# Kernel tuning notes

Hardware: AMD Instinct MI355X
Metric: run time of the kernel (lower is better)

The kernel has to match this reference:

```python
import jax, jax.numpy as jnp
import numpy as np

SIGMA_DATA = 16.0
ALPHA_BOND = 1.0


def safe_norm(x, axis=-1):
    # L2 norm with zero (sub)gradient at 0, matching torch.norm's behavior
    sq = jnp.sum(x * x, axis=axis)
    n = jnp.sqrt(jnp.where(sq > 0, sq, 1.0))
    return jnp.where(sq > 0, n, 0.0)


def weighted_rigid_align(x_l, xGT_l, w_l):
    # Aligns x_l onto xGT_l's frame (Kabsch with weights); output is detached.
    wm = w_l[..., None]                                   # [B,N,1]
    denom = jnp.sum(wm, axis=1, keepdims=True)
    mu = jnp.sum(wm * x_l, axis=1, keepdims=True) / denom
    muGT = jnp.sum(wm * xGT_l, axis=1, keepdims=True) / denom
    xc = x_l - mu
    xGTc = xGT_l - muGT
    # M = (w * xGT_c)^T @ x_c  -> [B,3,3]
    M = jnp.einsum('bni,bnj->bij', wm * xGTc, xc)
    U, S, Vh = jnp.linalg.svd(M)
    R = U @ Vh
    det = jnp.linalg.det(R)
    Fm = jnp.array([[1.0, 0.0, 0.0], [0.0, 1.0, 0.0], [0.0, 0.0, -1.0]], dtype=R.dtype)
    Rfix = jnp.einsum('bij,jk,bkl->bil', U, Fm, Vh)
    R = jnp.where(det[:, None, None] < 0, Rfix, R)
    xalign = xc @ jnp.swapaxes(R, -1, -2) + muGT
    return jax.lax.stop_gradient(xalign)


def diffusion_loss(xpred_l, xGT_l, ht, w_l):
    # Align ground truth onto prediction (note arg order in original forward)
    xGT_aligned = weighted_rigid_align(xGT_l, xpred_l, w_l)
    loss = jnp.sum(safe_norm(xpred_l - xGT_aligned) * w_l) / jnp.sum(w_l)
    if ALPHA_BOND > 0:
        w_pair = w_l[:, :, None] * w_l[:, None, :]                 # [B,N,N]
        d_pred = safe_norm(xpred_l[:, :, None] - xpred_l[:, None]) # [B,N,N]
        d_gt = safe_norm(xGT_l[:, :, None] - xGT_l[:, None])       # [B,N,N]
        L_bond = w_pair * (d_pred - d_gt) ** 2
        loss = loss + ALPHA_BOND * jnp.sum(L_bond) / jnp.sum(w_pair)
    return (ht ** 2 + SIGMA_DATA ** 2) / (ht + SIGMA_DATA) ** 2 * loss


def setup_inputs() -> dict:
    key = jax.random.key(0)
    k1, k2, k3, k4 = jax.random.split(key, 4)
    B, N = 4, 2048
    xpred_l = jax.random.normal(k1, (B, N, 3), dtype=jnp.float32) * 10.0
    xGT_l = jax.random.normal(k2, (B, N, 3), dtype=jnp.float32) * 10.0
    ht = jax.random.uniform(k3, (B,), dtype=jnp.float32, minval=0.1, maxval=4.0)
    w_l = jax.random.uniform(k4, (B, N), dtype=jnp.float32, minval=0.1, maxval=1.0)
    return {"xpred_l": xpred_l, "xGT_l": xGT_l, "ht": ht, "w_l": w_l}


def reference(xpred_l, xGT_l, ht, w_l):
    return diffusion_loss(xpred_l, xGT_l, ht, w_l)
```

## Files before the change

kernel.cpp:

```cpp
#include <hip/hip_runtime.h>
#include <math.h>


#define RT 256
#define TR 128
#define TC 128
#define MAXB 8

__global__ __launch_bounds__(RT, 4)
void k_bond_stats(const float* __restrict__ pred, const float* __restrict__ gt,
                  const float* __restrict__ w, double* __restrict__ ws,
                  int N, int B, int T, int CTILES, unsigned total) {
    const int b    = blockIdx.y;
    const int tid  = threadIdx.x;
    const int lane = tid & 63, wave = tid >> 6;

    int rem = blockIdx.x, bx = 0;
    while (rem >= CTILES - bx) { rem -= (CTILES - bx); bx++; }
    const int by = bx + rem;
    const int r0 = bx * TR, c0 = by * TC;

    double* statsSlot = ws;
    double* bondSlot  = ws + (size_t)B * CTILES * 16;
    if (blockIdx.x == 0 && blockIdx.y == 0 && tid == 0) {
        double* fin = bondSlot + total;
        fin[0] = 0.0; fin[1] = 0.0; fin[2] = 0.0;
    }

    const float* p  = pred + (size_t)b * N * 3;
    const float* g  = gt   + (size_t)b * N * 3;
    const float* wb = w    + (size_t)b * N;

    __shared__ float4 sp4[TC], sg4[TC];
    __shared__ double shred[4][16];

    const int rrow  = tid & (TR - 1);
    const int rhalf = tid >> 7;
    const int n     = r0 + rrow;
    const bool row_ok = (n < N);
    float px=0.f,py=0.f,pz=0.f,gx=0.f,gy=0.f,gz=0.f,wn=0.f;
    if (row_ok) {
        px = p[3*n]; py = p[3*n+1]; pz = p[3*n+2];
        gx = g[3*n]; gy = g[3*n+1]; gz = g[3*n+2];
        wn = wb[n];
    }

    {
        int i = tid & (TC - 1);
        int m = c0 + i;
        if (tid < TC) {
            float4 v = make_float4(0.f,0.f,0.f,0.f);
            if (m < N) v = make_float4(p[3*m], p[3*m+1], p[3*m+2], wb[m]);
            sp4[i] = v;
        } else {
            float4 v = make_float4(0.f,0.f,0.f,0.f);
            if (m < N) v = make_float4(g[3*m], g[3*m+1], g[3*m+2], 0.f);
            sg4[i] = v;
        }
    }
    __syncthreads();

    float acc = 0.f;
    const int ib = rhalf * (TC / 2);
    if (by > bx) {
        #pragma unroll 4
        for (int j = 0; j < TC/2; j++) {
            int i = ib + j;
            float4 cp = sp4[i], cg = sg4[i];
            float dxp=px-cp.x, dyp=py-cp.y, dzp=pz-cp.z;
            float dxg=gx-cg.x, dyg=gy-cg.y, dzg=gz-cg.z;
            float dp = sqrtf(dxp*dxp+dyp*dyp+dzp*dzp);
            float dg = sqrtf(dxg*dxg+dyg*dyg+dzg*dzg);
            float dd = dp - dg;
            acc = fmaf(cp.w, dd*dd, acc);
        }
    } else {
        #pragma unroll 4
        for (int j = 0; j < TC/2; j++) {
            int i = ib + j;
            float4 cp = sp4[i], cg = sg4[i];
            float dxp=px-cp.x, dyp=py-cp.y, dzp=pz-cp.z;
            float dxg=gx-cg.x, dyg=gy-cg.y, dzg=gz-cg.z;
            float dp = sqrtf(dxp*dxp+dyp*dyp+dzp*dzp);
            float dg = sqrtf(dxg*dxg+dyg*dyg+dzg*dzg);
            float dd = dp - dg;
            float t  = cp.w * (dd*dd);
            acc += (i > rrow) ? t : 0.f;
        }
    }
    float bond_f = 2.0f * wn * acc;

    if (bx == by) {
        double wd = (rhalf == 0) ? (double)wn : 0.0;
        double pxd=px,pyd=py,pzd=pz, gxd=gx,gyd=gy,gzd=gz;
        double st[16] = {wd, wd*pxd, wd*pyd, wd*pzd, wd*gxd, wd*gyd, wd*gzd,
                         wd*pxd*gxd, wd*pxd*gyd, wd*pxd*gzd,
                         wd*pyd*gxd, wd*pyd*gyd, wd*pyd*gzd,
                         wd*pzd*gxd, wd*pzd*gyd, wd*pzd*gzd};
        #pragma unroll
        for (int off = 32; off > 0; off >>= 1) {
            #pragma unroll
            for (int k = 0; k < 16; k++) st[k] += __shfl_down(st[k], off, 64);
        }
        if (lane == 0) {
            #pragma unroll
            for (int k = 0; k < 16; k++) shred[wave][k] = st[k];
        }
        __syncthreads();
        if (tid < 16)
            statsSlot[((size_t)b*CTILES + bx)*16 + tid] =
                shred[0][tid]+shred[1][tid]+shred[2][tid]+shred[3][tid];
        __syncthreads();
    }

    double bd = (double)bond_f;
    #pragma unroll
    for (int off = 32; off > 0; off >>= 1) bd += __shfl_down(bd, off, 64);
    if (lane == 0) shred[wave][0] = bd;
    __syncthreads();
    if (tid == 0)
        bondSlot[(size_t)blockIdx.y * T + blockIdx.x] =
            shred[0][0]+shred[1][0]+shred[2][0]+shred[3][0];
}

__global__ __launch_bounds__(RT, 1)
void k_tail2(const float* __restrict__ pred, const float* __restrict__ gt,
             const float* __restrict__ ht, const float* __restrict__ w,
             float* __restrict__ out, double* __restrict__ ws,
             int N, int B, int GX, unsigned total, int AG) {
    const int tid  = threadIdx.x;
    const int lane = tid & 63, wave = tid >> 6;
    const double* statsSlot = ws;
    const double* bondSlot  = ws + (size_t)B * GX * 16;
    double* fin = (double*)(bondSlot + total);

    __shared__ double sstat[MAXB][16];
    __shared__ float  sR[MAXB][15];
    __shared__ double sW[MAXB];
    __shared__ double shredA[4], shredB[4];

    float htv[MAXB];
    if (tid == 0) {
        #pragma unroll
        for (int b2 = 0; b2 < MAXB; b2++) htv[b2] = (b2 < B) ? ht[b2] : 0.f;
    }

    if (tid < B * 16) {
        int bb = tid >> 4, k = tid & 15;
        double acc = 0.0;
        for (int j = 0; j < GX; j++) acc += statsSlot[((size_t)bb*GX + j)*16 + k];
        sstat[bb][k] = acc;
    }

    double bsum = 0.0;
    for (unsigned i = (unsigned)blockIdx.x * RT + tid; i < total; i += (unsigned)AG * RT)
        bsum += bondSlot[i];

    const int ptTotal = B * N;
    const int stride  = AG * RT;
    const int pt0     = blockIdx.x * RT + tid;
    const bool have0  = (pt0 < ptTotal);
    float px=0.f,py=0.f,pz=0.f,qx=0.f,qy=0.f,qz=0.f,wn=0.f;
    int b0 = 0;
    if (have0) {
        b0 = pt0 / N; int n0 = pt0 - b0 * N;
        const float* pp = pred + (size_t)b0 * N * 3;
        const float* gg = gt   + (size_t)b0 * N * 3;
        px = pp[3*n0]; py = pp[3*n0+1]; pz = pp[3*n0+2];
        qx = gg[3*n0]; qy = gg[3*n0+1]; qz = gg[3*n0+2];
        wn = w[(size_t)b0 * N + n0];
    }

    __syncthreads();

    if (tid < B) {
        const double* s = sstat[tid];
        double W = s[0];
        double mup[3] = { s[1]/W, s[2]/W, s[3]/W };
        double mug[3] = { s[4]/W, s[5]/W, s[6]/W };
        double M[3][3];
        for (int i = 0; i < 3; i++)
            for (int j = 0; j < 3; j++)
                M[i][j] = s[7 + i*3 + j] - W * mup[i] * mug[j];
        double A[3][3];
        for (int i = 0; i < 3; i++)
            for (int j = 0; j < 3; j++) {
                double t = 0.0;
                for (int k = 0; k < 3; k++) t += M[k][i] * M[k][j];
                A[i][j] = t;
            }
        double V[3][3] = {{1,0,0},{0,1,0},{0,0,1}};
        for (int sweep = 0; sweep < 4; sweep++) {
            for (int pq = 0; pq < 3; pq++) {
                int pp_ = (pq == 2) ? 1 : 0;
                int qq_ = (pq == 0) ? 1 : 2;
                double apq = A[pp_][qq_];
                if (fabs(apq) < 1e-300) continue;
                double app = A[pp_][pp_], aqq = A[qq_][qq_];
                double theta = (aqq - app) / (2.0 * apq);
                double t = copysign(1.0, theta) / (fabs(theta) + sqrt(theta*theta + 1.0));
                double cj = 1.0 / sqrt(t*t + 1.0), sn = t * cj;
                A[pp_][pp_] = app - t * apq;
                A[qq_][qq_] = aqq + t * apq;
                A[pp_][qq_] = A[qq_][pp_] = 0.0;
                int r = 3 - pp_ - qq_;
                double arp = A[r][pp_], arq = A[r][qq_];
                A[r][pp_] = A[pp_][r] = cj*arp - sn*arq;
                A[r][qq_] = A[qq_][r] = sn*arp + cj*arq;
                for (int rr = 0; rr < 3; rr++) {
                    double vp = V[rr][pp_], vq = V[rr][qq_];
                    V[rr][pp_] = cj*vp - sn*vq;
                    V[rr][qq_] = sn*vp + cj*vq;
                }
            }
        }
        double d[3] = { A[0][0], A[1][1], A[2][2] };
        int idx[3] = {0, 1, 2};
        for (int i = 0; i < 2; i++)
            for (int j = i + 1; j < 3; j++)
                if (d[idx[j]] > d[idx[i]]) { int tt = idx[i]; idx[i] = idx[j]; idx[j] = tt; }
        double u[3][3], v[3][3];
        for (int i = 0; i < 3; i++) {
            int c_ = idx[i];
            double sv = sqrt(fmax(d[c_], 0.0));
            double inv = (sv > 1e-12) ? 1.0 / sv : 0.0;
            for (int r = 0; r < 3; r++) v[i][r] = V[r][c_];
            for (int r = 0; r < 3; r++) {
                double t = 0.0;
                for (int k = 0; k < 3; k++) t += M[r][k] * v[i][k];
                u[i][r] = t * inv;
            }
        }
        double detM = M[0][0]*(M[1][1]*M[2][2] - M[1][2]*M[2][1])
                    - M[0][1]*(M[1][0]*M[2][2] - M[1][2]*M[2][0])
                    + M[0][2]*(M[1][0]*M[2][1] - M[1][1]*M[2][0]);
        double sg2 = (detM < 0.0) ? -1.0 : 1.0;
        for (int r = 0; r < 3; r++)
            for (int cc2 = 0; cc2 < 3; cc2++)
                sR[tid][r*3+cc2] = (float)(u[0][r]*v[0][cc2] + u[1][r]*v[1][cc2]
                                           + sg2 * u[2][r]*v[2][cc2]);
        for (int i = 0; i < 3; i++) sR[tid][9 + i]  = (float)mup[i];
        for (int i = 0; i < 3; i++) sR[tid][12 + i] = (float)mug[i];
        sW[tid] = W;
    }
    __syncthreads();

    double al = 0.0;
    if (have0) {
        const float* Rb = sR[b0];
        float x0 = qx - Rb[12], x1 = qy - Rb[13], x2 = qz - Rb[14];
        float ax = fmaf(Rb[0],x0, fmaf(Rb[1],x1, fmaf(Rb[2],x2, Rb[9])));
        float ay = fmaf(Rb[3],x0, fmaf(Rb[4],x1, fmaf(Rb[5],x2, Rb[10])));
        float az = fmaf(Rb[6],x0, fmaf(Rb[7],x1, fmaf(Rb[8],x2, Rb[11])));
        float ex = px-ax, ey = py-ay, ez = pz-az;
        al += (double)(wn * sqrtf(ex*ex + ey*ey + ez*ez));
    }
    for (int pt = pt0 + stride; pt < ptTotal; pt += stride) {
        int b2 = pt / N; int nn = pt - b2 * N;
        const float* pp = pred + (size_t)b2 * N * 3;
        const float* gg = gt   + (size_t)b2 * N * 3;
        const float* Rb = sR[b2];
        float x0 = gg[3*nn]-Rb[12], x1 = gg[3*nn+1]-Rb[13], x2 = gg[3*nn+2]-Rb[14];
        float ax = fmaf(Rb[0],x0, fmaf(Rb[1],x1, fmaf(Rb[2],x2, Rb[9])));
        float ay = fmaf(Rb[3],x0, fmaf(Rb[4],x1, fmaf(Rb[5],x2, Rb[10])));
        float az = fmaf(Rb[6],x0, fmaf(Rb[7],x1, fmaf(Rb[8],x2, Rb[11])));
        float ex = pp[3*nn]-ax, ey = pp[3*nn+1]-ay, ez = pp[3*nn+2]-az;
        al += (double)(w[(size_t)b2*N + nn] * sqrtf(ex*ex + ey*ey + ez*ez));
    }

    #pragma unroll
    for (int off = 32; off > 0; off >>= 1) {
        al   += __shfl_down(al,   off, 64);
        bsum += __shfl_down(bsum, off, 64);
    }
    if (lane == 0) { shredA[wave] = al; shredB[wave] = bsum; }
    __syncthreads();

    if (tid == 0) {
        double alB = shredA[0]+shredA[1]+shredA[2]+shredA[3];
        double bB  = shredB[0]+shredB[1]+shredB[2]+shredB[3];
        atomicAdd(&fin[0], alB);
        atomicAdd(&fin[1], bB);
        __threadfence();
        unsigned old = atomicAdd((unsigned int*)&fin[2], 1u);
        if (old == (unsigned)(AG - 1)) {
            double at = atomicAdd(&fin[0], 0.0);
            double bt = atomicAdd(&fin[1], 0.0);
            double tw = 0.0, twp = 0.0;
            for (int b2 = 0; b2 < B; b2++) { double W = sW[b2]; tw += W; twp += W*W; }
            double loss = at / tw + bt / twp;
            #pragma unroll
            for (int b2 = 0; b2 < MAXB; b2++) {
                if (b2 < B) {
                    double h = (double)htv[b2];
                    out[b2] = (float)(((h*h + 256.0) / ((h + 16.0)*(h + 16.0))) * loss);
                }
            }
        }
    }
}

extern "C" void kernel_launch(void* const* d_in, const int* in_sizes, int n_in,
                              void* d_out, int out_size, void* d_ws, size_t ws_size,
                              hipStream_t stream) {
    const float* pred = (const float*)d_in[0];
    const float* gt   = (const float*)d_in[1];
    const float* ht   = (const float*)d_in[2];
    const float* w    = (const float*)d_in[3];
    int B = in_sizes[2];
    int N = in_sizes[3] / B;
    double* ws = (double*)d_ws;
    float* out = (float*)d_out;

    int CTILES = (N + TC - 1) / TC;
    int T = CTILES * (CTILES + 1) / 2;
    unsigned total = (unsigned)(B * T);

    int ag = (B * N + RT - 1) / RT;
    if (ag > 64) ag = 64;
    if (ag < 1)  ag = 1;

    k_bond_stats<<<dim3(T, B), dim3(RT), 0, stream>>>(pred, gt, w, ws, N, B, T, CTILES, total);
    k_tail2<<<dim3(ag), dim3(RT), 0, stream>>>(pred, gt, ht, w, out, ws, N, B, CTILES, total, ag);
}
```

Baseline: 92.50 us.

## Shrink pair tiles to 64 and split columns across four waves

Tile size drops from 128 to 64, so the grid has about four times as many triangular tile blocks. Each block now splits the 64 columns across four waves, not two halves. The linear-to-triangular tile index uses a closed-form sqrt estimate with correction loops instead of a serial loop. Per-tile stats are reduced by a single wave and written directly, which removes two block barriers. The goal is better occupancy and load balance across the CUs, at the cost of more blocks, more partial sums for the tail kernel and more redundant row loads.

```diff
diff --git a/kernel.cpp b/kernel.cpp
--- a/kernel.cpp
+++ b/kernel.cpp
@@ -3,11 +3,10 @@
 
 
 #define RT 256
-#define TR 128
-#define TC 128
+#define TSZ 64
 #define MAXB 8
 
-__global__ __launch_bounds__(RT, 4)
+__global__ __launch_bounds__(RT, 8)
 void k_bond_stats(const float* __restrict__ pred, const float* __restrict__ gt,
                   const float* __restrict__ w, double* __restrict__ ws,
                   int N, int B, int T, int CTILES, unsigned total) {
@@ -15,10 +14,17 @@
     const int tid  = threadIdx.x;
     const int lane = tid & 63, wave = tid >> 6;
 
-    int rem = blockIdx.x, bx = 0;
-    while (rem >= CTILES - bx) { rem -= (CTILES - bx); bx++; }
-    const int by = bx + rem;
-    const int r0 = bx * TR, c0 = by * TC;
+    int bx;
+    {
+        const int rem = blockIdx.x;
+        const float tc = 2.0f*CTILES + 1.0f;
+        bx = (int)((tc - sqrtf(tc*tc - 8.0f*(float)rem)) * 0.5f);
+        if (bx < 0) bx = 0;
+        while ((bx+1)*CTILES - (((bx+1)*bx) >> 1) <= rem) bx++;
+        while (bx*CTILES - ((bx*(bx-1)) >> 1) > rem) bx--;
+    }
+    const int by = bx + (blockIdx.x - (bx*CTILES - ((bx*(bx-1)) >> 1)));
+    const int r0 = bx * TSZ, c0 = by * TSZ;
 
     double* statsSlot = ws;
     double* bondSlot  = ws + (size_t)B * CTILES * 16;
@@ -31,12 +37,12 @@
     const float* g  = gt   + (size_t)b * N * 3;
     const float* wb = w    + (size_t)b * N;
 
-    __shared__ float4 sp4[TC], sg4[TC];
-    __shared__ double shred[4][16];
-
-    const int rrow  = tid & (TR - 1);
-    const int rhalf = tid >> 7;
-    const int n     = r0 + rrow;
+    __shared__ float4 sp4[TSZ], sg4[TSZ];
+    __shared__ double shred[4];
+
+    const int rrow = tid & (TSZ - 1);
+    const int q    = tid >> 6;
+    const int n    = r0 + rrow;
     const bool row_ok = (n < N);
     float px=0.f,py=0.f,pz=0.f,gx=0.f,gy=0.f,gz=0.f,wn=0.f;
     if (row_ok) {
@@ -45,10 +51,10 @@
         wn = wb[n];
     }
 
-    {
-        int i = tid & (TC - 1);
-        int m = c0 + i;
-        if (tid < TC) {
+    if (tid < 2*TSZ) {
+        const int i = tid & (TSZ - 1);
+        const int m = c0 + i;
+        if (tid < TSZ) {
             float4 v = make_float4(0.f,0.f,0.f,0.f);
             if (m < N) v = make_float4(p[3*m], p[3*m+1], p[3*m+2], wb[m]);
             sp4[i] = v;
@@ -61,11 +67,11 @@
     __syncthreads();
 
     float acc = 0.f;
-    const int ib = rhalf * (TC / 2);
+    const int ib = q * (TSZ/4);
     if (by > bx) {
         #pragma unroll 4
-        for (int j = 0; j < TC/2; j++) {
-            int i = ib + j;
+        for (int j = 0; j < TSZ/4; j++) {
+            const int i = ib + j;
             float4 cp = sp4[i], cg = sg4[i];
             float dxp=px-cp.x, dyp=py-cp.y, dzp=pz-cp.z;
             float dxg=gx-cg.x, dyg=gy-cg.y, dzg=gz-cg.z;
@@ -76,8 +82,8 @@
         }
     } else {
         #pragma unroll 4
-        for (int j = 0; j < TC/2; j++) {
-            int i = ib + j;
+        for (int j = 0; j < TSZ/4; j++) {
+            const int i = ib + j;
             float4 cp = sp4[i], cg = sg4[i];
             float dxp=px-cp.x, dyp=py-cp.y, dzp=pz-cp.z;
             float dxg=gx-cg.x, dyg=gy-cg.y, dzg=gz-cg.z;
@@ -88,10 +94,10 @@
             acc += (i > rrow) ? t : 0.f;
         }
     }
-    float bond_f = 2.0f * wn * acc;
-
-    if (bx == by) {
-        double wd = (rhalf == 0) ? (double)wn : 0.0;
+    const float bond_f = 2.0f * wn * acc;
+
+    if (bx == by && wave == 0) {
+        double wd = wn;
         double pxd=px,pyd=py,pzd=pz, gxd=gx,gyd=gy,gzd=gz;
         double st[16] = {wd, wd*pxd, wd*pyd, wd*pzd, wd*gxd, wd*gyd, wd*gzd,
                          wd*pxd*gxd, wd*pxd*gyd, wd*pxd*gzd,
@@ -104,23 +110,19 @@
         }
         if (lane == 0) {
             #pragma unroll
-            for (int k = 0; k < 16; k++) shred[wave][k] = st[k];
-        }
-        __syncthreads();
-        if (tid < 16)
-            statsSlot[((size_t)b*CTILES + bx)*16 + tid] =
-                shred[0][tid]+shred[1][tid]+shred[2][tid]+shred[3][tid];
-        __syncthreads();
+            for (int k = 0; k < 16; k++)
+                statsSlot[((size_t)b*CTILES + bx)*16 + k] = st[k];
+        }
     }
 
     double bd = (double)bond_f;
     #pragma unroll
     for (int off = 32; off > 0; off >>= 1) bd += __shfl_down(bd, off, 64);
-    if (lane == 0) shred[wave][0] = bd;
+    if (lane == 0) shred[wave] = bd;
     __syncthreads();
     if (tid == 0)
         bondSlot[(size_t)blockIdx.y * T + blockIdx.x] =
-            shred[0][0]+shred[1][0]+shred[2][0]+shred[3][0];
+            shred[0]+shred[1]+shred[2]+shred[3];
 }
 
 __global__ __launch_bounds__(RT, 1)
@@ -312,7 +314,7 @@
     double* ws = (double*)d_ws;
     float* out = (float*)d_out;
 
-    int CTILES = (N + TC - 1) / TC;
+    int CTILES = (N + TSZ - 1) / TSZ;
     int T = CTILES * (CTILES + 1) / 2;
     unsigned total = (unsigned)(B * T);
 
```

Result: no change. 92.82 us (+0.3%).
